# Performance work log

Measured on AMD Instinct MI355X. Metric: run time of the kernel, lower is better.

Reference implementation:

```python
import jax, jax.numpy as jnp
import numpy as np

S, B, I, H = 256, 512, 46, 256  # seqlen, batch, i_dim, h_dim
EPS = 1e-5


def setup_inputs() -> dict:
    key = jax.random.key(0)
    ks = iter(jax.random.split(key, 64))
    nrm = lambda shape, s=0.05: jax.random.normal(next(ks), shape, dtype=jnp.float32) * s
    inp = {}
    inp['X'] = jax.random.normal(next(ks), (S, B, I), dtype=jnp.float32)
    inp['M'] = (jax.random.uniform(next(ks), (S, B, I)) > 0.5).astype(jnp.float32)
    inp['mask'] = (jax.random.uniform(next(ks), (S, B)) > 0.1).astype(jnp.float32)
    C = I - 6  # 40 clinical channels
    inp['i2h_w'] = nrm((H, 6)); inp['i2h_b'] = nrm((H,))
    inp['comb_w'] = nrm((C, 2 * C)); inp['comb_b'] = nrm((C,))
    inp['down_w'] = nrm((H, C)); inp['down_b'] = nrm((H,))
    inp['conv1_w'] = nrm((H, C)); inp['conv1_b'] = nrm((H,))
    inp['conv2_w'] = nrm((H, H)); inp['conv2_b'] = nrm((H,))
    inp['bn1_g'] = jnp.ones((H,), jnp.float32); inp['bn1_b'] = jnp.zeros((H,), jnp.float32)
    inp['bn2_g'] = jnp.ones((H,), jnp.float32); inp['bn2_b'] = jnp.zeros((H,), jnp.float32)
    for p in ('r1', 'r2'):
        inp[p + '_wih'] = nrm((3 * H, H)); inp[p + '_whh'] = nrm((3 * H, H))
        inp[p + '_bih'] = nrm((3 * H,)); inp[p + '_bhh'] = nrm((3 * H,))
        inp[p + '_cw'] = nrm((H, 2 * H)); inp[p + '_cb'] = nrm((H,))
    inp['ln1_g'] = jnp.ones((H,), jnp.float32); inp['ln1_b'] = jnp.zeros((H,), jnp.float32)
    inp['ln2_g'] = jnp.ones((H,), jnp.float32); inp['ln2_b'] = jnp.zeros((H,), jnp.float32)
    inp['ln3_g'] = jnp.ones((8,), jnp.float32); inp['ln3_b'] = jnp.zeros((8,), jnp.float32)
    inp['nn1_w'] = nrm((8, H)); inp['nn1_b'] = nrm((8,))
    inp['nn2_w'] = nrm((2, 8)); inp['nn2_b'] = nrm((2,))
    return inp


def _bn(x, g, b):
    # BatchNorm1d in training mode: stats over (seq, batch) per channel, biased var
    mu = x.mean((0, 1))
    var = x.var((0, 1))
    return (x - mu) * jax.lax.rsqrt(var + EPS) * g + b


def _ln(x, g, b):
    mu = x.mean(-1, keepdims=True)
    var = x.var(-1, keepdims=True)
    return (x - mu) * jax.lax.rsqrt(var + EPS) * g + b


def _modgru(Xs, h0, mask, wih, whh, bih, bhh, cw, cb):
    # precompute input-gate projections for all timesteps: [S,B,3H]
    gi = jnp.einsum('sbi,gi->sbg', Xs, wih) + bih

    def step(h, inp):
        x, g, m = inp  # x:[B,H], g:[B,3H], m:[B]
        gh = h @ whh.T + bhh
        ir, iz, inn = jnp.split(g, 3, axis=-1)
        hr, hz, hn = jnp.split(gh, 3, axis=-1)
        r = jax.nn.sigmoid(ir + hr)
        z = jax.nn.sigmoid(iz + hz)
        n = jnp.tanh(inn + r * hn)
        h_new = (1.0 - z) * n + z * h  # GRUCell update
        mm = m[:, None]
        h = h_new * mm + h * (1.0 - mm)  # mask blend
        out = jnp.concatenate([x, h], axis=-1) @ cw.T + cb  # com2
        return h, out

    _, outs = jax.lax.scan(step, h0, (Xs, gi, mask))
    return outs


def reference(X, M, mask, i2h_w, i2h_b, comb_w, comb_b, down_w, down_b,
              conv1_w, conv1_b, conv2_w, conv2_b, bn1_g, bn1_b, bn2_g, bn2_b,
              r1_wih, r1_whh, r1_bih, r1_bhh, r1_cw, r1_cb,
              r2_wih, r2_whh, r2_bih, r2_bhh, r2_cw, r2_cb,
              ln1_g, ln1_b, ln2_g, ln2_b, ln3_g, ln3_b,
              nn1_w, nn1_b, nn2_w, nn2_b):
    p_info = X[0, :, -6:]          # [B,6] static patient info
    Xin = X[:, :, :-6]             # [S,B,40]
    Min = M[:, :, :-6]
    h0 = p_info @ i2h_w.T + i2h_b  # [B,H]
    res = Xin @ down_w.T + down_b  # [S,B,H]
    Xc = jnp.concatenate([Xin, Min], axis=-1) @ comb_w.T + comb_b
    # kernel-size-1 convs == per-timestep linear (layout kept [S,B,C])
    out = Xc @ conv1_w.T + conv1_b
    out = jax.nn.relu(_bn(out, bn1_g, bn1_b))
    out = out @ conv2_w.T + conv2_b
    out = _bn(out, bn2_g, bn2_b)
    hx = out + res
    hx = _ln(_modgru(hx, h0, mask, r1_wih, r1_whh, r1_bih, r1_bhh, r1_cw, r1_cb), ln1_g, ln1_b)
    hx = _ln(_modgru(hx, h0, mask, r2_wih, r2_whh, r2_bih, r2_bhh, r2_cw, r2_cb), ln2_g, ln2_b)
    hx = jax.nn.relu(hx @ nn1_w.T + nn1_b)
    hx = _ln(hx, ln3_g, ln3_b)
    return hx @ nn2_w.T + nn2_b  # [S,B,2]
```

## Files before the change

### kernel.cpp

```cpp
#include <hip/hip_runtime.h>
#include <hip/hip_bf16.h>

#define SS 256
#define BB 512
#define II 46
#define HH 256
#define CC 40
#define SB (SS*BB)
#define G3 (3*HH)
#define EPSF 1e-5f

typedef __attribute__((ext_vector_type(8))) short bf16x8;
typedef __attribute__((ext_vector_type(4))) float f32x4;

__device__ __forceinline__ unsigned short f2bf_rne(float f){
  unsigned u = __float_as_uint(f);
  unsigned r = (u + 0x7FFFu + ((u >> 16) & 1u)) >> 16;
  return (unsigned short)r;
}
__device__ __forceinline__ float bf2f(unsigned short b){
  return __uint_as_float(((unsigned)b) << 16);
}
__device__ __forceinline__ void cvt8(const float* v, bf16x8& hi, bf16x8& lo){
  #pragma unroll
  for (int e=0;e<8;e++){
    unsigned short hb = f2bf_rne(v[e]);
    hi[e] = (short)hb;
    lo[e] = (short)f2bf_rne(v[e] - bf2f(hb));
  }
}

__global__ void pack_xm_chunk_k(const float* __restrict__ X, const float* __restrict__ Mi,
                                float* __restrict__ XM, long long r0, int Rr){
  long long idx = (long long)blockIdx.x*blockDim.x + threadIdx.x;
  if (idx >= (long long)Rr*80) return;
  int r = (int)(idx / 80);
  int c = (int)(idx - (long long)r*80);
  long long gr = r0 + r;
  float v;
  if (c < CC) v = X[gr*II + c];
  else        v = Mi[gr*II + (c - CC)];
  XM[idx] = v;
}

__global__ void h0_k(const float* __restrict__ X, const float* __restrict__ w,
                     const float* __restrict__ bias, float* __restrict__ h1c,
                     float* __restrict__ h2c){
  int b = blockIdx.x, jj = threadIdx.x;
  const float* p = X + (long long)b*II + (II - 6);
  float acc = bias[jj];
  #pragma unroll
  for (int c2=0;c2<6;c2++) acc = fmaf(p[c2], w[jj*6 + c2], acc);
  h1c[(long long)b*HH + jj] = acc;
  h2c[(long long)b*HH + jj] = acc;
}

__global__ void whht_k(const float* __restrict__ w, float* __restrict__ wt){
  int idx = blockIdx.x*blockDim.x + threadIdx.x;
  if (idx >= G3*HH) return;
  int u = idx / HH, k = idx - u*HH;
  wt[(size_t)k*G3 + u] = w[idx];
}

template<int MODE>
__global__ void gemm_tn(const float* __restrict__ A, int lda,
                        const float* __restrict__ W, int ldw,
                        const float* __restrict__ bias,
                        float* __restrict__ Co, int ldc,
                        int Mrows, int N, int K)
{
  __shared__ __align__(16) float As[32][132];
  __shared__ __align__(16) float Ws[32][132];
  const int m0 = blockIdx.x*128, n0 = blockIdx.y*128;
  const int t  = threadIdx.x;
  const int tm = t >> 4, tn = t & 15;
  float acc[8][8];
  #pragma unroll
  for (int i=0;i<8;i++)
    #pragma unroll
    for (int j2=0;j2<8;j2++) acc[i][j2] = 0.f;

  for (int k0=0;k0<K;k0+=32){
    #pragma unroll
    for (int u=0;u<16;u++){
      int idx = u*256 + t;
      int r = idx >> 5, c = idx & 31;
      int gk = k0 + c;
      float av = 0.f, wv = 0.f;
      if (gk < K){
        int gm = m0 + r;
        if (gm < Mrows) av = A[(long long)gm*lda + gk];
        int gn = n0 + r;
        if (gn < N)     wv = W[(long long)gn*ldw + gk];
      }
      As[c][r] = av;
      Ws[c][r] = wv;
    }
    __syncthreads();
    #pragma unroll
    for (int kk=0;kk<32;kk++){
      const float4 a0 = *(const float4*)&As[kk][tm*8];
      const float4 a1 = *(const float4*)&As[kk][tm*8+4];
      const float4 b0 = *(const float4*)&Ws[kk][tn*8];
      const float4 b1 = *(const float4*)&Ws[kk][tn*8+4];
      const float av[8] = {a0.x,a0.y,a0.z,a0.w,a1.x,a1.y,a1.z,a1.w};
      const float bv[8] = {b0.x,b0.y,b0.z,b0.w,b1.x,b1.y,b1.z,b1.w};
      #pragma unroll
      for (int i=0;i<8;i++)
        #pragma unroll
        for (int j2=0;j2<8;j2++) acc[i][j2] = fmaf(av[i], bv[j2], acc[i][j2]);
    }
    __syncthreads();
  }
  #pragma unroll
  for (int i=0;i<8;i++){
    int gm = m0 + tm*8 + i;
    if (gm < Mrows){
      #pragma unroll
      for (int j2=0;j2<8;j2++){
        int gn = n0 + tn*8 + j2;
        if (gn < N){
          long long oi = (long long)gm*ldc + gn;
          float val = acc[i][j2] + bias[gn];
          if (MODE == 1) val = fmaxf(val, 0.f);
          if (MODE == 2) val += Co[oi];
          Co[oi] = val;
        }
      }
    }
  }
}

template<int MODE>
__global__ __launch_bounds__(256) void gemm_mf(
    const float* __restrict__ A, int lda,
    const float* __restrict__ W, int ldw,
    const float* __restrict__ bias,
    float* __restrict__ Co, int ldc,
    int N, int K)
{
  __shared__ __align__(16) unsigned short Ah[128*32];
  __shared__ __align__(16) unsigned short Al[128*32];
  __shared__ __align__(16) unsigned short Bh[128*32];
  __shared__ __align__(16) unsigned short Bl[128*32];
  const int t = threadIdx.x;
  const int m0 = blockIdx.x*128, n0 = blockIdx.y*128;
  const int lane = t & 63, w = t >> 6;
  const int wm = (w & 1)*64, wn = (w >> 1)*64;
  const int fr = lane & 15, fg = lane >> 4;

  f32x4 acc[4][4];
  #pragma unroll
  for (int i=0;i<4;i++)
    #pragma unroll
    for (int j=0;j<4;j++){ f32x4 z; z[0]=0;z[1]=0;z[2]=0;z[3]=0; acc[i][j]=z; }

  for (int k0=0; k0<K; k0+=32){
    #pragma unroll
    for (int cc=0; cc<2; cc++){
      const int c   = t + cc*256;
      const int row = c >> 2, kg = c & 3;
      const int byte = row*64 + ((kg*16) ^ (((row>>1)&3)<<4));
      {
        const float* ap = A + (size_t)(m0+row)*lda + k0 + kg*8;
        float v[8];
        *(float4*)&v[0] = *(const float4*)ap;
        *(float4*)&v[4] = *(const float4*)(ap+4);
        bf16x8 hi, lo; cvt8(v, hi, lo);
        *(bf16x8*)((char*)Ah + byte) = hi;
        *(bf16x8*)((char*)Al + byte) = lo;
      }
      {
        const float* bp = W + (size_t)(n0+row)*ldw + k0 + kg*8;
        float v[8];
        *(float4*)&v[0] = *(const float4*)bp;
        *(float4*)&v[4] = *(const float4*)(bp+4);
        bf16x8 hi, lo; cvt8(v, hi, lo);
        *(bf16x8*)((char*)Bh + byte) = hi;
        *(bf16x8*)((char*)Bl + byte) = lo;
      }
    }
    __syncthreads();
    bf16x8 ahi[4], alo[4], bhi[4], blo[4];
    #pragma unroll
    for (int mt=0; mt<4; mt++){
      const int r = wm + mt*16 + fr;
      const int byte = r*64 + ((fg*16) ^ (((r>>1)&3)<<4));
      ahi[mt] = *(const bf16x8*)((const char*)Ah + byte);
      alo[mt] = *(const bf16x8*)((const char*)Al + byte);
    }
    #pragma unroll
    for (int nt=0; nt<4; nt++){
      const int r = wn + nt*16 + fr;
      const int byte = r*64 + ((fg*16) ^ (((r>>1)&3)<<4));
      bhi[nt] = *(const bf16x8*)((const char*)Bh + byte);
      blo[nt] = *(const bf16x8*)((const char*)Bl + byte);
    }
    #pragma unroll
    for (int mt=0; mt<4; mt++)
      #pragma unroll
      for (int nt=0; nt<4; nt++){
        acc[mt][nt] = __builtin_amdgcn_mfma_f32_16x16x32_bf16(alo[mt], bhi[nt], acc[mt][nt], 0,0,0);
        acc[mt][nt] = __builtin_amdgcn_mfma_f32_16x16x32_bf16(ahi[mt], blo[nt], acc[mt][nt], 0,0,0);
        acc[mt][nt] = __builtin_amdgcn_mfma_f32_16x16x32_bf16(ahi[mt], bhi[nt], acc[mt][nt], 0,0,0);
      }
    __syncthreads();
  }

  #pragma unroll
  for (int mt=0; mt<4; mt++){
    #pragma unroll
    for (int nt=0; nt<4; nt++){
      const int col = n0 + wn + nt*16 + fr;
      const float bv = bias[col];
      #pragma unroll
      for (int i=0;i<4;i++){
        const int row = m0 + wm + mt*16 + fg*4 + i;
        const size_t oi = (size_t)row*ldc + col;
        float val = acc[mt][nt][i] + bv;
        if (MODE == 2) val += Co[oi];
        Co[oi] = val;
      }
    }
  }
}

__global__ __launch_bounds__(256) void gemm_mf_dual(
    const float* __restrict__ A1, const float* __restrict__ A2,
    const float* __restrict__ W,
    const float* __restrict__ bias,
    float* __restrict__ Co, int ldc, int N)
{
  __shared__ __align__(16) unsigned short Ah[128*32];
  __shared__ __align__(16) unsigned short Al[128*32];
  __shared__ __align__(16) unsigned short Bh[128*32];
  __shared__ __align__(16) unsigned short Bl[128*32];
  const int t = threadIdx.x;
  const int m0 = blockIdx.x*128, n0 = blockIdx.y*128;
  const int lane = t & 63, w = t >> 6;
  const int wm = (w & 1)*64, wn = (w >> 1)*64;
  const int fr = lane & 15, fg = lane >> 4;

  f32x4 acc[4][4];
  #pragma unroll
  for (int i=0;i<4;i++)
    #pragma unroll
    for (int j=0;j<4;j++){ f32x4 z; z[0]=0;z[1]=0;z[2]=0;z[3]=0; acc[i][j]=z; }

  for (int k0=0; k0<2*HH; k0+=32){
    const float* Abase = (k0 < HH) ? A1 : A2;
    const int    kofs  = (k0 < HH) ? k0 : (k0 - HH);
    #pragma unroll
    for (int cc=0; cc<2; cc++){
      const int c   = t + cc*256;
      const int row = c >> 2, kg = c & 3;
      const int byte = row*64 + ((kg*16) ^ (((row>>1)&3)<<4));
      {
        const float* ap = Abase + (size_t)(m0+row)*HH + kofs + kg*8;
        float v[8];
        *(float4*)&v[0] = *(const float4*)ap;
        *(float4*)&v[4] = *(const float4*)(ap+4);
        bf16x8 hi, lo; cvt8(v, hi, lo);
        *(bf16x8*)((char*)Ah + byte) = hi;
        *(bf16x8*)((char*)Al + byte) = lo;
      }
      {
        const float* bp = W + (size_t)(n0+row)*(2*HH) + k0 + kg*8;
        float v[8];
        *(float4*)&v[0] = *(const float4*)bp;
        *(float4*)&v[4] = *(const float4*)(bp+4);
        bf16x8 hi, lo; cvt8(v, hi, lo);
        *(bf16x8*)((char*)Bh + byte) = hi;
        *(bf16x8*)((char*)Bl + byte) = lo;
      }
    }
    __syncthreads();
    bf16x8 ahi[4], alo[4], bhi[4], blo[4];
    #pragma unroll
    for (int mt=0; mt<4; mt++){
      const int r = wm + mt*16 + fr;
      const int byte = r*64 + ((fg*16) ^ (((r>>1)&3)<<4));
      ahi[mt] = *(const bf16x8*)((const char*)Ah + byte);
      alo[mt] = *(const bf16x8*)((const char*)Al + byte);
    }
    #pragma unroll
    for (int nt=0; nt<4; nt++){
      const int r = wn + nt*16 + fr;
      const int byte = r*64 + ((fg*16) ^ (((r>>1)&3)<<4));
      bhi[nt] = *(const bf16x8*)((const char*)Bh + byte);
      blo[nt] = *(const bf16x8*)((const char*)Bl + byte);
    }
    #pragma unroll
    for (int mt=0; mt<4; mt++)
      #pragma unroll
      for (int nt=0; nt<4; nt++){
        acc[mt][nt] = __builtin_amdgcn_mfma_f32_16x16x32_bf16(alo[mt], bhi[nt], acc[mt][nt], 0,0,0);
        acc[mt][nt] = __builtin_amdgcn_mfma_f32_16x16x32_bf16(ahi[mt], blo[nt], acc[mt][nt], 0,0,0);
        acc[mt][nt] = __builtin_amdgcn_mfma_f32_16x16x32_bf16(ahi[mt], bhi[nt], acc[mt][nt], 0,0,0);
      }
    __syncthreads();
  }

  #pragma unroll
  for (int mt=0; mt<4; mt++){
    #pragma unroll
    for (int nt=0; nt<4; nt++){
      const int col = n0 + wn + nt*16 + fr;
      const float bv = bias[col];
      #pragma unroll
      for (int i=0;i<4;i++){
        const int row = m0 + wm + mt*16 + fg*4 + i;
        const size_t oi = (size_t)row*ldc + col;
        Co[oi] = acc[mt][nt][i] + bv;
      }
    }
  }
}

__global__ void bn_partial_k(const float* __restrict__ Xc, float* __restrict__ ps,
                             float* __restrict__ pq, int pblk0){
  int blk = blockIdx.x, t = threadIdx.x;
  long long base = (long long)blk*512*HH;
  float s = 0.f, q = 0.f;
  for (int r=0;r<512;r++){
    float v = Xc[base + (long long)r*HH + t];
    s += v; q = fmaf(v, v, q);
  }
  ps[(pblk0+blk)*HH + t] = s;
  pq[(pblk0+blk)*HH + t] = q;
}

__global__ void bn_final_k(const float* __restrict__ ps, const float* __restrict__ pq,
                           const float* __restrict__ g, const float* __restrict__ b,
                           float* __restrict__ sc, float* __restrict__ sh){
  int t = threadIdx.x;
  double s = 0.0, q = 0.0;
  for (int i=0;i<256;i++){ s += (double)ps[i*HH + t]; q += (double)pq[i*HH + t]; }
  double mu  = s / (double)SB;
  double var = q / (double)SB - mu*mu;
  float scv = (float)((double)g[t] / sqrt(var + 1e-5));
  sc[t] = scv;
  sh[t] = (float)((double)b[t] - mu*(double)scv);
}

__global__ void fold_k(const float* __restrict__ w, const float* __restrict__ b,
                       const float* __restrict__ sc, const float* __restrict__ sh,
                       float* __restrict__ wf, float* __restrict__ bf, int K){
  int idx = blockIdx.x*blockDim.x + threadIdx.x;
  if (idx < 256*K){ int o = idx / K; wf[idx] = w[idx]*sc[o]; }
  if (idx < 256)  bf[idx] = b[idx]*sc[idx] + sh[idx];
}

__global__ void ln_rows_k(const float* __restrict__ Xi, float* __restrict__ Xo,
                          const float* __restrict__ g, const float* __restrict__ b){
  long long row = blockIdx.x;
  int t = threadIdx.x;
  float v = Xi[row*HH + t];
  float s = v, q = v*v;
  #pragma unroll
  for (int o=32;o>0;o>>=1){ s += __shfl_down(s,o); q += __shfl_down(q,o); }
  __shared__ float ssm[4], qqm[4];
  int w = t >> 6;
  if ((t & 63) == 0){ ssm[w] = s; qqm[w] = q; }
  __syncthreads();
  if (t == 0){ ssm[0] = ssm[0]+ssm[1]+ssm[2]+ssm[3]; qqm[0] = qqm[0]+qqm[1]+qqm[2]+qqm[3]; }
  __syncthreads();
  s = ssm[0]; q = qqm[0];
  float mu  = s * (1.f/HH);
  float var = q * (1.f/HH) - mu*mu;
  float rs  = rsqrtf(var + EPSF);
  Xo[row*HH + t] = (v - mu)*rs*g[t] + b[t];
}

#define DOT4(hv,A0,A1,A2,A3) \
  A0=fmaf(hv.x,w0.x,A0); A0=fmaf(hv.y,w1.x,A0); A0=fmaf(hv.z,w2.x,A0); A0=fmaf(hv.w,w3.x,A0); \
  A1=fmaf(hv.x,w0.y,A1); A1=fmaf(hv.y,w1.y,A1); A1=fmaf(hv.z,w2.y,A1); A1=fmaf(hv.w,w3.y,A1); \
  A2=fmaf(hv.x,w0.z,A2); A2=fmaf(hv.y,w1.z,A2); A2=fmaf(hv.z,w2.z,A2); A2=fmaf(hv.w,w3.z,A2); \
  A3=fmaf(hv.x,w0.w,A3); A3=fmaf(hv.y,w1.w,A3); A3=fmaf(hv.z,w2.w,A3); A3=fmaf(hv.w,w3.w,A3);

__global__ __launch_bounds__(768) void gru_scan_fused_k(
  const float* __restrict__ gi1, const float* __restrict__ w1T,
  const float* __restrict__ b1v, const float* __restrict__ m1v,
  float* __restrict__ hc1, float* __restrict__ Hh1o, int nst1,
  const float* __restrict__ gi2, const float* __restrict__ w2T,
  const float* __restrict__ b2v, const float* __restrict__ m2v,
  float* __restrict__ hc2, float* __restrict__ Hh2o, int nst2)
{
  const int gsel = blockIdx.x & 1;
  const int blk  = blockIdx.x >> 1;
  const float* gi    = gsel ? gi2 : gi1;
  const float* whhT  = gsel ? w2T : w1T;
  const float* bhh   = gsel ? b2v : b1v;
  const float* mask0 = gsel ? m2v : m1v;
  float* hcar        = gsel ? hc2 : hc1;
  float* Hh          = gsel ? Hh2o : Hh1o;
  const int nst      = gsel ? nst2 : nst1;
  if (nst <= 0) return;

  const int t  = threadIdx.x;
  const int b0 = blk*4;
  const int cg = t % 192;
  const int ks = t / 192;
  const int c0 = cg*4;
  const int k0 = ks*64;
  __shared__ __align__(16) float h[4][260];
  __shared__ __align__(16) float part[4][4][776];
  __shared__ float mkz[4];

  const int uj = t & 255;
  const int ur = t >> 8;
  if (t < 512){
    h[ur  ][uj] = hcar[(size_t)(b0+ur  )*HH + uj];
    h[ur+2][uj] = hcar[(size_t)(b0+ur+2)*HH + uj];
  }
  float br=0.f, bz=0.f, bn_=0.f;
  if (t < 512){ br = bhh[uj]; bz = bhh[uj+HH]; bn_ = bhh[uj+2*HH]; }
  __syncthreads();

  const float* wbase = whhT + (size_t)k0*G3 + c0;

  for (int st=0; st<nst; ++st){
    float i0r=0,i0z=0,i0n=0, i1r=0,i1z=0,i1n=0;
    if (t < 512){
      const size_t ga = ((size_t)st*BB + b0 + ur  )*G3 + uj;
      const size_t gb = ((size_t)st*BB + b0 + ur+2)*G3 + uj;
      i0r=gi[ga]; i0z=gi[ga+HH]; i0n=gi[ga+2*HH];
      i1r=gi[gb]; i1z=gi[gb+HH]; i1n=gi[gb+2*HH];
    }
    if (t < 4) mkz[t] = mask0[(size_t)st*BB + b0 + t];

    float a00=0,a01=0,a02=0,a03=0;
    float a10=0,a11=0,a12=0,a13=0;
    float a20=0,a21=0,a22=0,a23=0;
    float a30=0,a31=0,a32=0,a33=0;
    #pragma unroll 4
    for (int kk=0; kk<64; kk+=4){
      const float4 w0 = *(const float4*)(wbase + (size_t)(kk  )*G3);
      const float4 w1 = *(const float4*)(wbase + (size_t)(kk+1)*G3);
      const float4 w2 = *(const float4*)(wbase + (size_t)(kk+2)*G3);
      const float4 w3 = *(const float4*)(wbase + (size_t)(kk+3)*G3);
      const float4 h0 = *(const float4*)&h[0][k0+kk];
      const float4 h1 = *(const float4*)&h[1][k0+kk];
      const float4 h2 = *(const float4*)&h[2][k0+kk];
      const float4 h3 = *(const float4*)&h[3][k0+kk];
      DOT4(h0,a00,a01,a02,a03);
      DOT4(h1,a10,a11,a12,a13);
      DOT4(h2,a20,a21,a22,a23);
      DOT4(h3,a30,a31,a32,a33);
    }
    *(float4*)&part[ks][0][c0] = make_float4(a00,a01,a02,a03);
    *(float4*)&part[ks][1][c0] = make_float4(a10,a11,a12,a13);
    *(float4*)&part[ks][2][c0] = make_float4(a20,a21,a22,a23);
    *(float4*)&part[ks][3][c0] = make_float4(a30,a31,a32,a33);
    __syncthreads();

    if (t < 512){
      {
        const int r_ = ur;
        const float ar = part[0][r_][uj]+part[1][r_][uj]+part[2][r_][uj]+part[3][r_][uj] + br;
        const float az = part[0][r_][uj+HH]+part[1][r_][uj+HH]+part[2][r_][uj+HH]+part[3][r_][uj+HH] + bz;
        const float an = part[0][r_][uj+2*HH]+part[1][r_][uj+2*HH]+part[2][r_][uj+2*HH]+part[3][r_][uj+2*HH] + bn_;
        const float rr = 1.f/(1.f + __expf(-(i0r + ar)));
        const float zz = 1.f/(1.f + __expf(-(i0z + az)));
        const float nn = tanhf(fmaf(rr, an, i0n));
        const float hold = h[r_][uj];
        const float m = mkz[r_];
        const float hnew = (1.f - zz)*nn + zz*hold;
        const float hv = hnew*m + hold*(1.f - m);
        h[r_][uj] = hv;
        Hh[((size_t)st*BB + b0 + r_)*HH + uj] = hv;
      }
      {
        const int r_ = ur + 2;
        const float ar = part[0][r_][uj]+part[1][r_][uj]+part[2][r_][uj]+part[3][r_][uj] + br;
        const float az = part[0][r_][uj+HH]+part[1][r_][uj+HH]+part[2][r_][uj+HH]+part[3][r_][uj+HH] + bz;
        const float an = part[0][r_][uj+2*HH]+part[1][r_][uj+2*HH]+part[2][r_][uj+2*HH]+part[3][r_][uj+2*HH] + bn_;
        const float rr = 1.f/(1.f + __expf(-(i1r + ar)));
        const float zz = 1.f/(1.f + __expf(-(i1z + az)));
        const float nn = tanhf(fmaf(rr, an, i1n));
        const float hold = h[r_][uj];
        const float m = mkz[r_];
        const float hnew = (1.f - zz)*nn + zz*hold;
        const float hv = hnew*m + hold*(1.f - m);
        h[r_][uj] = hv;
        Hh[((size_t)st*BB + b0 + r_)*HH + uj] = hv;
      }
    }
    __syncthreads();
  }
  if (t < 512){
    hcar[(size_t)(b0+ur  )*HH + uj] = h[ur  ][uj];
    hcar[(size_t)(b0+ur+2)*HH + uj] = h[ur+2][uj];
  }
}

__global__ void head_ln_k(const float* __restrict__ hx,
                          const float* __restrict__ g2, const float* __restrict__ b2,
                          const float* __restrict__ w1, const float* __restrict__ b1,
                          const float* __restrict__ g3, const float* __restrict__ b3,
                          const float* __restrict__ w2, const float* __restrict__ b2h,
                          float* __restrict__ outp, long long r0){
  long long row = blockIdx.x;
  int t = threadIdx.x;
  float v = hx[row*HH + t];
  float s = v, q = v*v;
  #pragma unroll
  for (int o=32;o>0;o>>=1){ s += __shfl_down(s,o); q += __shfl_down(q,o); }
  __shared__ float ssm[4], qqm[4];
  int w = t >> 6;
  if ((t & 63) == 0){ ssm[w] = s; qqm[w] = q; }
  __syncthreads();
  if (t == 0){ ssm[0] = ssm[0]+ssm[1]+ssm[2]+ssm[3]; qqm[0] = qqm[0]+qqm[1]+qqm[2]+qqm[3]; }
  __syncthreads();
  s = ssm[0]; q = qqm[0];
  float mu  = s * (1.f/HH);
  float var = q * (1.f/HH) - mu*mu;
  float rs  = rsqrtf(var + EPSF);
  __shared__ float xs[HH];
  xs[t] = (v - mu)*rs*g2[t] + b2[t];
  __syncthreads();
  int o = t >> 5, l = t & 31;
  const float* wv = w1 + o*HH;
  float acc = 0.f;
  for (int k=l;k<HH;k+=32) acc = fmaf(xs[k], wv[k], acc);
  #pragma unroll
  for (int d=16;d>0;d>>=1) acc += __shfl_down(acc, d, 32);
  __shared__ float a8[8];
  if (l == 0) a8[o] = fmaxf(acc + b1[o], 0.f);
  __syncthreads();
  if (t == 0){
    float ss = 0.f;
    #pragma unroll
    for (int i=0;i<8;i++) ss += a8[i];
    float m8 = ss*0.125f;
    float qq = 0.f;
    #pragma unroll
    for (int i=0;i<8;i++){ float d = a8[i]-m8; qq = fmaf(d,d,qq); }
    float r8 = rsqrtf(qq*0.125f + EPSF);
    float y0 = b2h[0], y1 = b2h[1];
    #pragma unroll
    for (int i=0;i<8;i++){
      float vv = (a8[i]-m8)*r8*g3[i] + b3[i];
      y0 = fmaf(vv, w2[i],   y0);
      y1 = fmaf(vv, w2[8+i], y1);
    }
    outp[(r0+row)*2+0] = y0; outp[(r0+row)*2+1] = y1;
  }
}

extern "C" void kernel_launch(void* const* d_in, const int* in_sizes, int n_in,
                              void* d_out, int out_size, void* d_ws, size_t ws_size,
                              hipStream_t stream) {
  const float* X      = (const float*)d_in[0];
  const float* Mi     = (const float*)d_in[1];
  const float* mask   = (const float*)d_in[2];
  const float* i2h_w  = (const float*)d_in[3];
  const float* i2h_b  = (const float*)d_in[4];
  const float* comb_w = (const float*)d_in[5];
  const float* comb_b = (const float*)d_in[6];
  const float* down_w = (const float*)d_in[7];
  const float* down_b = (const float*)d_in[8];
  const float* conv1_w= (const float*)d_in[9];
  const float* conv1_b= (const float*)d_in[10];
  const float* conv2_w= (const float*)d_in[11];
  const float* conv2_b= (const float*)d_in[12];
  const float* bn1_g  = (const float*)d_in[13];
  const float* bn1_b  = (const float*)d_in[14];
  const float* bn2_g  = (const float*)d_in[15];
  const float* bn2_b  = (const float*)d_in[16];
  const float* r1_wih = (const float*)d_in[17];
  const float* r1_whh = (const float*)d_in[18];
  const float* r1_bih = (const float*)d_in[19];
  const float* r1_bhh = (const float*)d_in[20];
  const float* r1_cw  = (const float*)d_in[21];
  const float* r1_cb  = (const float*)d_in[22];
  const float* r2_wih = (const float*)d_in[23];
  const float* r2_whh = (const float*)d_in[24];
  const float* r2_bih = (const float*)d_in[25];
  const float* r2_bhh = (const float*)d_in[26];
  const float* r2_cw  = (const float*)d_in[27];
  const float* r2_cb  = (const float*)d_in[28];
  const float* ln1_g  = (const float*)d_in[29];
  const float* ln1_b  = (const float*)d_in[30];
  const float* ln2_g  = (const float*)d_in[31];
  const float* ln2_b  = (const float*)d_in[32];
  const float* ln3_g  = (const float*)d_in[33];
  const float* ln3_b  = (const float*)d_in[34];
  const float* nn1_w  = (const float*)d_in[35];
  const float* nn1_b  = (const float*)d_in[36];
  const float* nn2_w  = (const float*)d_in[37];
  const float* nn2_b  = (const float*)d_in[38];
  float* outp = (float*)d_out;

  const size_t tail_floats = 2*(size_t)BB*HH + 2*(size_t)256*HH + 2*HH
                           + (size_t)256*40 + 256 + (size_t)HH*HH + 256
                           + 2*(size_t)G3*HH + (size_t)SB*CC;
  int cands[6] = {256,128,64,32,16,8};
  int sc_chunk = 0;
  for (int ci=0; ci<6; ci++){
    size_t R = (size_t)512*cands[ci];
    size_t need = (R*2816 + tail_floats)*sizeof(float);
    if (need <= ws_size){ sc_chunk = cands[ci]; break; }
  }
  if (!sc_chunk) return;

  const size_t R = (size_t)512*sc_chunk;
  const int Ri = (int)R;
  const int nchunks = SB / Ri;

  float* wsf = (float*)d_ws;
  float* A   = wsf;
  float* GI1 = A + R*HH;
  float* GI2 = GI1 + R*G3;
  float* Cxp = GI2 + R*G3;
  float* Ee  = Cxp + R*HH;
  float* Hh2 = Ee + R*HH;
  float* Hx1 = Hh2 + R*HH;
  float* tl  = Hx1 + R*HH;
  float* H1C = tl;
  float* H2C = H1C + (size_t)BB*HH;
  float* PS  = H2C + (size_t)BB*HH;
  float* PQ  = PS  + (size_t)256*HH;
  float* SCv = PQ  + (size_t)256*HH;
  float* SHv = SCv + HH;
  float* W1F = SHv + HH;
  float* B1F = W1F + (size_t)256*40;
  float* W2F = B1F + HH;
  float* B2F = W2F + (size_t)HH*HH;
  float* W1T = B2F + HH;
  float* W2T = W1T + (size_t)HH*G3;
  float* XcF = W2T + (size_t)HH*G3;

  whht_k<<<(G3*HH + 255)/256, 256, 0, stream>>>(r1_whh, W1T);
  whht_k<<<(G3*HH + 255)/256, 256, 0, stream>>>(r2_whh, W2T);

  const int PACKG = (Ri*80 + 255)/256;
  const int MB = Ri/128;

  for (int c=0;c<nchunks;c++){
    long long r0 = (long long)c*R;
    pack_xm_chunk_k<<<PACKG, 256, 0, stream>>>(X, Mi, Ee, r0, Ri);
    gemm_tn<0><<<dim3(MB,1), 256, 0, stream>>>(Ee, 80, comb_w, 80, comb_b, XcF + r0*CC, CC, Ri, CC, 80);
    gemm_tn<0><<<dim3(MB,2), 256, 0, stream>>>(XcF + r0*CC, CC, conv1_w, CC, conv1_b, Ee, HH, Ri, HH, CC);
    bn_partial_k<<<Ri/512, 256, 0, stream>>>(Ee, PS, PQ, (int)(r0/512));
  }
  bn_final_k<<<1, 256, 0, stream>>>(PS, PQ, bn1_g, bn1_b, SCv, SHv);
  fold_k<<<(256*40 + 255)/256, 256, 0, stream>>>(conv1_w, conv1_b, SCv, SHv, W1F, B1F, 40);

  for (int c=0;c<nchunks;c++){
    long long r0 = (long long)c*R;
    gemm_tn<1><<<dim3(MB,2), 256, 0, stream>>>(XcF + r0*CC, CC, W1F, CC, B1F, Ee, HH, Ri, HH, CC);
    gemm_mf<0><<<dim3(MB,2), 256, 0, stream>>>(Ee, HH, conv2_w, HH, conv2_b, A, HH, HH, HH);
    bn_partial_k<<<Ri/512, 256, 0, stream>>>(A, PS, PQ, (int)(r0/512));
  }
  bn_final_k<<<1, 256, 0, stream>>>(PS, PQ, bn2_g, bn2_b, SCv, SHv);
  fold_k<<<(256*256 + 255)/256, 256, 0, stream>>>(conv2_w, conv2_b, SCv, SHv, W2F, B2F, 256);

  h0_k<<<BB, HH, 0, stream>>>(X, i2h_w, i2h_b, H1C, H2C);

  for (int c=0;c<nchunks;c++){
    long long r0 = (long long)c*R;
    long long rp = r0 - (long long)R;
    gemm_tn<0><<<dim3(MB,2), 256, 0, stream>>>(X + r0*II, II, down_w, CC, down_b, A, HH, Ri, HH, CC);
    gemm_tn<1><<<dim3(MB,2), 256, 0, stream>>>(XcF + r0*CC, CC, W1F, CC, B1F, Ee, HH, Ri, HH, CC);
    gemm_mf<2><<<dim3(MB,2), 256, 0, stream>>>(Ee, HH, W2F, HH, B2F, A, HH, HH, HH);
    gemm_mf<0><<<dim3(MB,6), 256, 0, stream>>>(A, HH, r1_wih, HH, r1_bih, GI1, G3, G3, HH);
    gru_scan_fused_k<<<2*(BB/4), 768, 0, stream>>>(
        GI1, W1T, r1_bhh, mask + r0, H1C, Ee, sc_chunk,
        GI2, W2T, r2_bhh, (c > 0) ? (mask + rp) : mask, H2C, Hh2, (c > 0) ? sc_chunk : 0);
    if (c > 0){
      gemm_mf_dual<<<dim3(MB,2), 256, 0, stream>>>(Hx1, Hh2, r2_cw, r2_cb, Cxp, HH, HH);
      head_ln_k<<<Ri, 256, 0, stream>>>(Cxp, ln2_g, ln2_b, nn1_w, nn1_b, ln3_g, ln3_b, nn2_w, nn2_b, outp, rp);
    }
    gemm_mf_dual<<<dim3(MB,2), 256, 0, stream>>>(A, Ee, r1_cw, r1_cb, Cxp, HH, HH);
    ln_rows_k<<<Ri, 256, 0, stream>>>(Cxp, Hx1, ln1_g, ln1_b);
    gemm_mf<0><<<dim3(MB,6), 256, 0, stream>>>(Hx1, HH, r2_wih, HH, r2_bih, GI2, G3, G3, HH);
  }
  {
    long long rl = (long long)(nchunks-1)*R;
    gru_scan_fused_k<<<2*(BB/4), 768, 0, stream>>>(
        GI1, W1T, r1_bhh, mask, H1C, Ee, 0,
        GI2, W2T, r2_bhh, mask + rl, H2C, Hh2, sc_chunk);
    gemm_mf_dual<<<dim3(MB,2), 256, 0, stream>>>(Hx1, Hh2, r2_cw, r2_cb, Cxp, HH, HH);
    head_ln_k<<<Ri, 256, 0, stream>>>(Cxp, ln2_g, ln2_b, nn1_w, nn1_b, ln3_g, ln3_b, nn2_w, nn2_b, outp, rl);
  }
}
```

Baseline: 6.660 ms.

## Pre-split GEMM weights to bf16 hi/lo, fuse X/M pack, widen BN partials

```diff
diff --git a/kernel.cpp b/kernel.cpp
--- a/kernel.cpp
+++ b/kernel.cpp
@@ -9,6 +9,7 @@
 #define SB (SS*BB)
 #define G3 (3*HH)
 #define EPSF 1e-5f
+#define NPART (SB/64)
 
 typedef __attribute__((ext_vector_type(8))) short bf16x8;
 typedef __attribute__((ext_vector_type(4))) float f32x4;
@@ -30,17 +31,14 @@
   }
 }
 
-__global__ void pack_xm_chunk_k(const float* __restrict__ X, const float* __restrict__ Mi,
-                                float* __restrict__ XM, long long r0, int Rr){
-  long long idx = (long long)blockIdx.x*blockDim.x + threadIdx.x;
-  if (idx >= (long long)Rr*80) return;
-  int r = (int)(idx / 80);
-  int c = (int)(idx - (long long)r*80);
-  long long gr = r0 + r;
-  float v;
-  if (c < CC) v = X[gr*II + c];
-  else        v = Mi[gr*II + (c - CC)];
-  XM[idx] = v;
+__global__ void split_w_k(const float* __restrict__ w, unsigned short* __restrict__ wh,
+                          unsigned short* __restrict__ wl, int n){
+  int i = blockIdx.x*256 + threadIdx.x;
+  if (i >= n) return;
+  float v = w[i];
+  unsigned short hb = f2bf_rne(v);
+  wh[i] = hb;
+  wl[i] = f2bf_rne(v - bf2f(hb));
 }
 
 __global__ void h0_k(const float* __restrict__ X, const float* __restrict__ w,
@@ -62,12 +60,13 @@
   wt[(size_t)k*G3 + u] = w[idx];
 }
 
-template<int MODE>
+template<int MODE, int XM>
 __global__ void gemm_tn(const float* __restrict__ A, int lda,
                         const float* __restrict__ W, int ldw,
                         const float* __restrict__ bias,
                         float* __restrict__ Co, int ldc,
-                        int Mrows, int N, int K)
+                        int Mrows, int N, int K,
+                        const float* __restrict__ A2, long long r0)
 {
   __shared__ __align__(16) float As[32][132];
   __shared__ __align__(16) float Ws[32][132];
@@ -89,7 +88,14 @@
       float av = 0.f, wv = 0.f;
       if (gk < K){
         int gm = m0 + r;
-        if (gm < Mrows) av = A[(long long)gm*lda + gk];
+        if (gm < Mrows){
+          if (XM){
+            long long gr = r0 + gm;
+            av = (gk < CC) ? A[gr*II + gk] : A2[gr*II + (gk - CC)];
+          } else {
+            av = A[(long long)gm*lda + gk];
+          }
+        }
         int gn = n0 + r;
         if (gn < N)     wv = W[(long long)gn*ldw + gk];
       }
@@ -132,9 +138,9 @@
 }
 
 template<int MODE>
-__global__ __launch_bounds__(256) void gemm_mf(
+__global__ __launch_bounds__(256) void gemm_mfp(
     const float* __restrict__ A, int lda,
-    const float* __restrict__ W, int ldw,
+    const unsigned short* __restrict__ Wh, const unsigned short* __restrict__ Wl, int ldw,
     const float* __restrict__ bias,
     float* __restrict__ Co, int ldc,
     int N, int K)
@@ -171,13 +177,9 @@
         *(bf16x8*)((char*)Al + byte) = lo;
       }
       {
-        const float* bp = W + (size_t)(n0+row)*ldw + k0 + kg*8;
-        float v[8];
-        *(float4*)&v[0] = *(const float4*)bp;
-        *(float4*)&v[4] = *(const float4*)(bp+4);
-        bf16x8 hi, lo; cvt8(v, hi, lo);
-        *(bf16x8*)((char*)Bh + byte) = hi;
-        *(bf16x8*)((char*)Bl + byte) = lo;
+        const size_t off = (size_t)(n0+row)*ldw + k0 + kg*8;
+        *(bf16x8*)((char*)Bh + byte) = *(const bf16x8*)&Wh[off];
+        *(bf16x8*)((char*)Bl + byte) = *(const bf16x8*)&Wl[off];
       }
     }
     __syncthreads();
@@ -225,9 +227,9 @@
   }
 }
 
-__global__ __launch_bounds__(256) void gemm_mf_dual(
+__global__ __launch_bounds__(256) void gemm_mfp_dual(
     const float* __restrict__ A1, const float* __restrict__ A2,
-    const float* __restrict__ W,
+    const unsigned short* __restrict__ Wh, const unsigned short* __restrict__ Wl,
     const float* __restrict__ bias,
     float* __restrict__ Co, int ldc, int N)
 {
@@ -265,13 +267,9 @@
         *(bf16x8*)((char*)Al + byte) = lo;
       }
       {
-        const float* bp = W + (size_t)(n0+row)*(2*HH) + k0 + kg*8;
-        float v[8];
-        *(float4*)&v[0] = *(const float4*)bp;
-        *(float4*)&v[4] = *(const float4*)(bp+4);
-        bf16x8 hi, lo; cvt8(v, hi, lo);
-        *(bf16x8*)((char*)Bh + byte) = hi;
-        *(bf16x8*)((char*)Bl + byte) = lo;
+        const size_t off = (size_t)(n0+row)*(2*HH) + k0 + kg*8;
+        *(bf16x8*)((char*)Bh + byte) = *(const bf16x8*)&Wh[off];
+        *(bf16x8*)((char*)Bl + byte) = *(const bf16x8*)&Wl[off];
       }
     }
     __syncthreads();
@@ -320,14 +318,14 @@
 __global__ void bn_partial_k(const float* __restrict__ Xc, float* __restrict__ ps,
                              float* __restrict__ pq, int pblk0){
   int blk = blockIdx.x, t = threadIdx.x;
-  long long base = (long long)blk*512*HH;
+  long long base = (long long)blk*64*HH;
   float s = 0.f, q = 0.f;
-  for (int r=0;r<512;r++){
+  for (int r=0;r<64;r++){
     float v = Xc[base + (long long)r*HH + t];
     s += v; q = fmaf(v, v, q);
   }
-  ps[(pblk0+blk)*HH + t] = s;
-  pq[(pblk0+blk)*HH + t] = q;
+  ps[(size_t)(pblk0+blk)*HH + t] = s;
+  pq[(size_t)(pblk0+blk)*HH + t] = q;
 }
 
 __global__ void bn_final_k(const float* __restrict__ ps, const float* __restrict__ pq,
@@ -335,7 +333,7 @@
                            float* __restrict__ sc, float* __restrict__ sh){
   int t = threadIdx.x;
   double s = 0.0, q = 0.0;
-  for (int i=0;i<256;i++){ s += (double)ps[i*HH + t]; q += (double)pq[i*HH + t]; }
+  for (int i=0;i<NPART;i++){ s += (double)ps[(size_t)i*HH + t]; q += (double)pq[(size_t)i*HH + t]; }
   double mu  = s / (double)SB;
   double var = q / (double)SB - mu*mu;
   float scv = (float)((double)g[t] / sqrt(var + 1e-5));
@@ -592,14 +590,17 @@
   const float* nn2_b  = (const float*)d_in[38];
   float* outp = (float*)d_out;
 
-  const size_t tail_floats = 2*(size_t)BB*HH + 2*(size_t)256*HH + 2*HH
+  const size_t us_elems = 2*((size_t)HH*HH + (size_t)HH*HH + (size_t)G3*HH
+                           + (size_t)G3*HH + (size_t)HH*2*HH + (size_t)HH*2*HH);
+  const size_t tail_floats = 2*(size_t)BB*HH + 2*(size_t)NPART*HH + 2*HH
                            + (size_t)256*40 + 256 + (size_t)HH*HH + 256
-                           + 2*(size_t)G3*HH + (size_t)SB*CC;
+                           + 2*(size_t)G3*HH + (size_t)SB*CC
+                           + (us_elems + 1)/2;
   int cands[6] = {256,128,64,32,16,8};
   int sc_chunk = 0;
   for (int ci=0; ci<6; ci++){
     size_t R = (size_t)512*cands[ci];
-    size_t need = (R*2816 + tail_floats)*sizeof(float);
+    size_t need = (R*2560 + tail_floats)*sizeof(float);
     if (need <= ws_size){ sc_chunk = cands[ci]; break; }
   }
   if (!sc_chunk) return;
@@ -611,17 +612,17 @@
   float* wsf = (float*)d_ws;
   float* A   = wsf;
   float* GI1 = A + R*HH;
+  float* Cxp = GI1;
   float* GI2 = GI1 + R*G3;
-  float* Cxp = GI2 + R*G3;
-  float* Ee  = Cxp + R*HH;
+  float* Ee  = GI2 + R*G3;
   float* Hh2 = Ee + R*HH;
   float* Hx1 = Hh2 + R*HH;
   float* tl  = Hx1 + R*HH;
   float* H1C = tl;
   float* H2C = H1C + (size_t)BB*HH;
   float* PS  = H2C + (size_t)BB*HH;
-  float* PQ  = PS  + (size_t)256*HH;
-  float* SCv = PQ  + (size_t)256*HH;
+  float* PQ  = PS  + (size_t)NPART*HH;
+  float* SCv = PQ  + (size_t)NPART*HH;
   float* SHv = SCv + HH;
   float* W1F = SHv + HH;
   float* B1F = W1F + (size_t)256*40;
@@ -630,58 +631,75 @@
   float* W1T = B2F + HH;
   float* W2T = W1T + (size_t)HH*G3;
   float* XcF = W2T + (size_t)HH*G3;
+  unsigned short* usb = (unsigned short*)(XcF + (size_t)SB*CC);
+  unsigned short* C2H  = usb;
+  unsigned short* C2L  = C2H  + (size_t)HH*HH;
+  unsigned short* W2FH = C2L  + (size_t)HH*HH;
+  unsigned short* W2FL = W2FH + (size_t)HH*HH;
+  unsigned short* WI1H = W2FL + (size_t)HH*HH;
+  unsigned short* WI1L = WI1H + (size_t)G3*HH;
+  unsigned short* WI2H = WI1L + (size_t)G3*HH;
+  unsigned short* WI2L = WI2H + (size_t)G3*HH;
+  unsigned short* CW1H = WI2L + (size_t)G3*HH;
+  unsigned short* CW1L = CW1H + (size_t)HH*2*HH;
+  unsigned short* CW2H = CW1L + (size_t)HH*2*HH;
+  unsigned short* CW2L = CW2H + (size_t)HH*2*HH;
 
   whht_k<<<(G3*HH + 255)/256, 256, 0, stream>>>(r1_whh, W1T);
   whht_k<<<(G3*HH + 255)/256, 256, 0, stream>>>(r2_whh, W2T);
-
-  const int PACKG = (Ri*80 + 255)/256;
+  split_w_k<<<(HH*HH + 255)/256, 256, 0, stream>>>(conv2_w, C2H, C2L, HH*HH);
+  split_w_k<<<(G3*HH + 255)/256, 256, 0, stream>>>(r1_wih, WI1H, WI1L, G3*HH);
+  split_w_k<<<(G3*HH + 255)/256, 256, 0, stream>>>(r2_wih, WI2H, WI2L, G3*HH);
+  split_w_k<<<(HH*2*HH + 255)/256, 256, 0, stream>>>(r1_cw, CW1H, CW1L, HH*2*HH);
+  split_w_k<<<(HH*2*HH + 255)/256, 256, 0, stream>>>(r2_cw, CW2H, CW2L, HH*2*HH);
+
   const int MB = Ri/128;
 
   for (int c=0;c<nchunks;c++){
     long long r0 = (long long)c*R;
-    pack_xm_chunk_k<<<PACKG, 256, 0, stream>>>(X, Mi, Ee, r0, Ri);
-    gemm_tn<0><<<dim3(MB,1), 256, 0, stream>>>(Ee, 80, comb_w, 80, comb_b, XcF + r0*CC, CC, Ri, CC, 80);
-    gemm_tn<0><<<dim3(MB,2), 256, 0, stream>>>(XcF + r0*CC, CC, conv1_w, CC, conv1_b, Ee, HH, Ri, HH, CC);
-    bn_partial_k<<<Ri/512, 256, 0, stream>>>(Ee, PS, PQ, (int)(r0/512));
+    gemm_tn<0,1><<<dim3(MB,1), 256, 0, stream>>>(X, II, comb_w, 80, comb_b, XcF + r0*CC, CC, Ri, CC, 80, Mi, r0);
+    gemm_tn<0,0><<<dim3(MB,2), 256, 0, stream>>>(XcF + r0*CC, CC, conv1_w, CC, conv1_b, Ee, HH, Ri, HH, CC, nullptr, 0);
+    bn_partial_k<<<Ri/64, 256, 0, stream>>>(Ee, PS, PQ, (int)(r0/64));
   }
   bn_final_k<<<1, 256, 0, stream>>>(PS, PQ, bn1_g, bn1_b, SCv, SHv);
   fold_k<<<(256*40 + 255)/256, 256, 0, stream>>>(conv1_w, conv1_b, SCv, SHv, W1F, B1F, 40);
 
   for (int c=0;c<nchunks;c++){
     long long r0 = (long long)c*R;
-    gemm_tn<1><<<dim3(MB,2), 256, 0, stream>>>(XcF + r0*CC, CC, W1F, CC, B1F, Ee, HH, Ri, HH, CC);
-    gemm_mf<0><<<dim3(MB,2), 256, 0, stream>>>(Ee, HH, conv2_w, HH, conv2_b, A, HH, HH, HH);
-    bn_partial_k<<<Ri/512, 256, 0, stream>>>(A, PS, PQ, (int)(r0/512));
+    gemm_tn<1,0><<<dim3(MB,2), 256, 0, stream>>>(XcF + r0*CC, CC, W1F, CC, B1F, Ee, HH, Ri, HH, CC, nullptr, 0);
+    gemm_mfp<0><<<dim3(MB,2), 256, 0, stream>>>(Ee, HH, C2H, C2L, HH, conv2_b, A, HH, HH, HH);
+    bn_partial_k<<<Ri/64, 256, 0, stream>>>(A, PS, PQ, (int)(r0/64));
   }
   bn_final_k<<<1, 256, 0, stream>>>(PS, PQ, bn2_g, bn2_b, SCv, SHv);
   fold_k<<<(256*256 + 255)/256, 256, 0, stream>>>(conv2_w, conv2_b, SCv, SHv, W2F, B2F, 256);
+  split_w_k<<<(HH*HH + 255)/256, 256, 0, stream>>>(W2F, W2FH, W2FL, HH*HH);
 
   h0_k<<<BB, HH, 0, stream>>>(X, i2h_w, i2h_b, H1C, H2C);
 
   for (int c=0;c<nchunks;c++){
     long long r0 = (long long)c*R;
     long long rp = r0 - (long long)R;
-    gemm_tn<0><<<dim3(MB,2), 256, 0, stream>>>(X + r0*II, II, down_w, CC, down_b, A, HH, Ri, HH, CC);
-    gemm_tn<1><<<dim3(MB,2), 256, 0, stream>>>(XcF + r0*CC, CC, W1F, CC, B1F, Ee, HH, Ri, HH, CC);
-    gemm_mf<2><<<dim3(MB,2), 256, 0, stream>>>(Ee, HH, W2F, HH, B2F, A, HH, HH, HH);
-    gemm_mf<0><<<dim3(MB,6), 256, 0, stream>>>(A, HH, r1_wih, HH, r1_bih, GI1, G3, G3, HH);
+    gemm_tn<0,0><<<dim3(MB,2), 256, 0, stream>>>(X + r0*II, II, down_w, CC, down_b, A, HH, Ri, HH, CC, nullptr, 0);
+    gemm_tn<1,0><<<dim3(MB,2), 256, 0, stream>>>(XcF + r0*CC, CC, W1F, CC, B1F, Ee, HH, Ri, HH, CC, nullptr, 0);
+    gemm_mfp<2><<<dim3(MB,2), 256, 0, stream>>>(Ee, HH, W2FH, W2FL, HH, B2F, A, HH, HH, HH);
+    gemm_mfp<0><<<dim3(MB,6), 256, 0, stream>>>(A, HH, WI1H, WI1L, HH, r1_bih, GI1, G3, G3, HH);
     gru_scan_fused_k<<<2*(BB/4), 768, 0, stream>>>(
         GI1, W1T, r1_bhh, mask + r0, H1C, Ee, sc_chunk,
         GI2, W2T, r2_bhh, (c > 0) ? (mask + rp) : mask, H2C, Hh2, (c > 0) ? sc_chunk : 0);
     if (c > 0){
-      gemm_mf_dual<<<dim3(MB,2), 256, 0, stream>>>(Hx1, Hh2, r2_cw, r2_cb, Cxp, HH, HH);
+      gemm_mfp_dual<<<dim3(MB,2), 256, 0, stream>>>(Hx1, Hh2, CW2H, CW2L, r2_cb, Cxp, HH, HH);
       head_ln_k<<<Ri, 256, 0, stream>>>(Cxp, ln2_g, ln2_b, nn1_w, nn1_b, ln3_g, ln3_b, nn2_w, nn2_b, outp, rp);
     }
-    gemm_mf_dual<<<dim3(MB,2), 256, 0, stream>>>(A, Ee, r1_cw, r1_cb, Cxp, HH, HH);
+    gemm_mfp_dual<<<dim3(MB,2), 256, 0, stream>>>(A, Ee, CW1H, CW1L, r1_cb, Cxp, HH, HH);
     ln_rows_k<<<Ri, 256, 0, stream>>>(Cxp, Hx1, ln1_g, ln1_b);
-    gemm_mf<0><<<dim3(MB,6), 256, 0, stream>>>(Hx1, HH, r2_wih, HH, r2_bih, GI2, G3, G3, HH);
+    gemm_mfp<0><<<dim3(MB,6), 256, 0, stream>>>(Hx1, HH, WI2H, WI2L, HH, r2_bih, GI2, G3, G3, HH);
   }
   {
     long long rl = (long long)(nchunks-1)*R;
     gru_scan_fused_k<<<2*(BB/4), 768, 0, stream>>>(
         GI1, W1T, r1_bhh, mask, H1C, Ee, 0,
         GI2, W2T, r2_bhh, mask + rl, H2C, Hh2, sc_chunk);
-    gemm_mf_dual<<<dim3(MB,2), 256, 0, stream>>>(Hx1, Hh2, r2_cw, r2_cb, Cxp, HH, HH);
+    gemm_mfp_dual<<<dim3(MB,2), 256, 0, stream>>>(Hx1, Hh2, CW2H, CW2L, r2_cb, Cxp, HH, HH);
     head_ln_k<<<Ri, 256, 0, stream>>>(Cxp, ln2_g, ln2_b, nn1_w, nn1_b, ln3_g, ln3_b, nn2_w, nn2_b, outp, rl);
   }
 }
```

New measurement: 6.738 ms. About the same (+1.2%).
